# Optimization experiments

Measured on AMD Instinct MI355X. Metric: run time of the kernel, lower is better.

The kernel has to match this reference:

```python
import jax, jax.numpy as jnp
import numpy as np

N = 50000      # nodes
E = 400000     # edges
F = 64         # feature_size
H = 4          # heads
D = 16         # embedding_size (per-head dim)
HD = H * D     # concat hidden = 64
ED = 16        # edge_dim
L = 3          # model_layers (extra TransformerConv layers)
DN = 256       # dense_neurons
G = 128        # number of graphs in the batch
SCALE = float(1.0 / np.sqrt(D))


def setup_inputs() -> dict:
    key = jax.random.key(0)
    ks = jax.random.split(key, 40)

    def w(k, shape, fan_in):
        return jax.random.normal(k, shape, jnp.float32) / np.float32(np.sqrt(fan_in))

    inp = {}
    inp["x"] = jax.random.normal(ks[0], (N, F), jnp.float32)
    inp["edge_attr"] = jax.random.normal(ks[1], (E, ED), jnp.float32)
    inp["edge_index"] = jax.random.randint(ks[2], (2, E), 0, N)
    inp["batch"] = jnp.sort(jax.random.randint(ks[3], (N,), 0, G))

    # conv1: feature_size -> heads*embedding
    inp["Wq0"] = w(ks[4], (F, HD), F); inp["bq0"] = jnp.zeros((HD,), jnp.float32)
    inp["Wk0"] = w(ks[5], (F, HD), F); inp["bk0"] = jnp.zeros((HD,), jnp.float32)
    inp["Wv0"] = w(ks[6], (F, HD), F); inp["bv0"] = jnp.zeros((HD,), jnp.float32)
    inp["We0"] = w(ks[7], (ED, HD), ED)                      # lin_edge, no bias
    inp["Ws0"] = w(ks[8], (F, HD), F); inp["bs0"] = jnp.zeros((HD,), jnp.float32)  # lin_skip
    inp["Wb0"] = w(ks[9], (3 * HD, 1), 3 * HD)               # lin_beta, no bias

    # stacked layers 1..L: heads*embedding -> heads*embedding
    inp["Wq"] = w(ks[10], (L, HD, HD), HD); inp["bq"] = jnp.zeros((L, HD), jnp.float32)
    inp["Wk"] = w(ks[11], (L, HD, HD), HD); inp["bk"] = jnp.zeros((L, HD), jnp.float32)
    inp["Wv"] = w(ks[12], (L, HD, HD), HD); inp["bv"] = jnp.zeros((L, HD), jnp.float32)
    inp["We"] = w(ks[13], (L, ED, HD), ED)
    inp["Ws"] = w(ks[14], (L, HD, HD), HD); inp["bs"] = jnp.zeros((L, HD), jnp.float32)
    inp["Wb"] = w(ks[15], (L, 3 * HD, 1), 3 * HD)

    # MLP head: Linear(2*HD -> DN), Linear(DN -> 1)
    inp["Wlin"] = w(ks[16], (2 * HD, DN), 2 * HD); inp["blin"] = jnp.zeros((DN,), jnp.float32)
    inp["Wout"] = w(ks[17], (DN, 1), DN); inp["bout"] = jnp.zeros((1,), jnp.float32)
    return inp


def _tconv(x, edge_attr, src, dst, Wq, bq, Wk, bk, Wv, bv, We, Ws, bs, Wb):
    """PyG TransformerConv (concat=True, beta=True, edge_dim), eval mode (no dropout)."""
    n = x.shape[0]
    q = (x @ Wq + bq).reshape(n, H, D)
    k = (x @ Wk + bk).reshape(n, H, D)
    v = (x @ Wv + bv).reshape(n, H, D)
    e = (edge_attr @ We).reshape(-1, H, D)
    ke = k[src] + e                                   # [E,H,D] keys with edge feats
    ve = v[src] + e                                   # [E,H,D] values with edge feats
    logits = jnp.einsum('ehd,ehd->eh', q[dst], ke) * SCALE
    # segment softmax over incoming edges of each target node
    m = jax.ops.segment_max(logits, dst, num_segments=n)
    p = jnp.exp(logits - m[dst])
    s = jax.ops.segment_sum(p, dst, num_segments=n)
    a = p / (s[dst] + 1e-16)                          # [E,H]
    agg = jax.ops.segment_sum(a[:, :, None] * ve, dst, num_segments=n).reshape(n, HD)
    skip = x @ Ws + bs                                # root/skip transform
    beta = jax.nn.sigmoid(jnp.concatenate([agg, skip, agg - skip], axis=-1) @ Wb)
    return beta * skip + (1.0 - beta) * agg


def reference(x, edge_attr, edge_index, batch,
              Wq0, bq0, Wk0, bk0, Wv0, bv0, We0, Ws0, bs0, Wb0,
              Wq, bq, Wk, bk, Wv, bv, We, Ws, bs, Wb,
              Wlin, blin, Wout, bout):
    src, dst = edge_index[0], edge_index[1]
    h = jax.nn.relu(_tconv(x, edge_attr, src, dst,
                           Wq0, bq0, Wk0, bk0, Wv0, bv0, We0, Ws0, bs0, Wb0))
    for i in range(L):
        h = jax.nn.relu(_tconv(h, edge_attr, src, dst,
                               Wq[i], bq[i], Wk[i], bk[i], Wv[i], bv[i],
                               We[i], Ws[i], bs[i], Wb[i]))
    # global max pool (gmp) and global mean pool (gap)
    cnt = jax.ops.segment_sum(jnp.ones((h.shape[0],), h.dtype), batch, num_segments=G)
    gmax = jax.ops.segment_max(h, batch, num_segments=G)
    gmax = jnp.where(cnt[:, None] > 0, gmax, 0.0)
    gmean = jax.ops.segment_sum(h, batch, num_segments=G) / jnp.maximum(cnt[:, None], 1.0)
    z = jnp.concatenate([gmax, gmean], axis=-1) @ Wlin + blin
    return jax.nn.sigmoid(z @ Wout + bout)
```

## Files before the change

### kernel.cpp

```cpp
#include <hip/hip_runtime.h>
#include <math.h>

#define SCALEF 0.25f
#define LOG2E  1.4426950408889634f

typedef __attribute__((ext_vector_type(8))) short short8;
typedef __attribute__((ext_vector_type(4))) float f32x4;

__device__ __forceinline__ unsigned short f2bf(float x) {
  unsigned u = __float_as_uint(x);
  unsigned r = u + 0x7FFFu + ((u >> 16) & 1u);
  return (unsigned short)(r >> 16);
}
__device__ __forceinline__ float bf2f(unsigned short h) {
  return __uint_as_float(((unsigned)h) << 16);
}

__global__ void k_hist(const int* __restrict__ dst, int* __restrict__ counts, int E) {
  int i = blockIdx.x * 256 + threadIdx.x;
  if (i < E) atomicAdd(&counts[dst[i]], 1);
}

__global__ __launch_bounds__(1024) void k_scan1(const int* __restrict__ counts,
                                                int* __restrict__ excl,
                                                int* __restrict__ bsums, int n) {
  __shared__ int sd[1024];
  int t = threadIdx.x;
  int i = blockIdx.x * 1024 + t;
  int v = (i < n) ? counts[i] : 0;
  sd[t] = v;
  __syncthreads();
  for (int off = 1; off < 1024; off <<= 1) {
    int x = (t >= off) ? sd[t - off] : 0;
    __syncthreads();
    sd[t] += x;
    __syncthreads();
  }
  if (i < n) excl[i] = sd[t] - v;
  if (t == 1023) bsums[blockIdx.x] = sd[1023];
}

__global__ __launch_bounds__(64) void k_scan2(int* bsums, int nb) {
  const int lane = threadIdx.x;
  int v = (lane < nb) ? bsums[lane] : 0;
  const int orig = v;
  for (int off = 1; off < 64; off <<= 1) {
    int u = __shfl_up(v, off, 64);
    if (lane >= off) v += u;
  }
  if (lane < nb) bsums[lane] = v - orig;
}

__global__ __launch_bounds__(1024) void k_scan3(int* __restrict__ rowptr, int* __restrict__ cursor,
                                                const int* __restrict__ bsums, int n, int Etot) {
  int i = blockIdx.x * 1024 + threadIdx.x;
  if (i < n) { int v = rowptr[i] + bsums[blockIdx.x]; rowptr[i] = v; cursor[i] = v; }
  if (i == 0) rowptr[n] = Etot;
}

__global__ void k_scatperm(const int* __restrict__ esrc, const int* __restrict__ edst,
                           const float* __restrict__ EA, int* __restrict__ cursor,
                           int* __restrict__ esrcp, unsigned short* __restrict__ EAp, int E) {
  int i = blockIdx.x * 256 + threadIdx.x;
  if (i >= E) return;
  const int pos = atomicAdd(&cursor[edst[i]], 1);
  esrcp[pos] = esrc[i] * 256;
  const float4* s4 = (const float4*)(EA + ((size_t)i << 4));
  float4 a = s4[0], b = s4[1], c = s4[2], d = s4[3];
  union { unsigned short us[16]; uint4 u4[2]; } o;
  o.us[0] = f2bf(a.x); o.us[1] = f2bf(a.y); o.us[2] = f2bf(a.z); o.us[3] = f2bf(a.w);
  o.us[4] = f2bf(b.x); o.us[5] = f2bf(b.y); o.us[6] = f2bf(b.z); o.us[7] = f2bf(b.w);
  o.us[8] = f2bf(c.x); o.us[9] = f2bf(c.y); o.us[10] = f2bf(c.z); o.us[11] = f2bf(c.w);
  o.us[12] = f2bf(d.x); o.us[13] = f2bf(d.y); o.us[14] = f2bf(d.z); o.us[15] = f2bf(d.w);
  uint4* d4 = (uint4*)(EAp + ((size_t)pos << 4));
  d4[0] = o.u4[0]; d4[1] = o.u4[1];
}

__global__ __launch_bounds__(256) void k_wqt(
    const float* __restrict__ Wq0, const float* __restrict__ bq0, const float* __restrict__ We0,
    const float* __restrict__ Wq, const float* __restrict__ bq, const float* __restrict__ We,
    float* __restrict__ Wqt, float* __restrict__ bqt) {
  const int l = blockIdx.x;
  const float* wq = (l == 0) ? Wq0 : Wq + (l - 1) * 4096;
  const float* bv = (l == 0) ? bq0 : bq + (l - 1) * 64;
  const float* we = (l == 0) ? We0 : We + (l - 1) * 1024;
  float* out  = Wqt + l * 4096;
  float* outb = bqt + l * 64;
  const int t = threadIdx.x;
  const int r = t >> 2;
  const int hh = t & 3;
  float wqr[16];
  #pragma unroll
  for (int d = 0; d < 16; ++d) wqr[d] = wq[r * 64 + hh * 16 + d];
  #pragma unroll
  for (int bb = 0; bb < 16; ++bb) {
    float s = 0.f;
    #pragma unroll
    for (int d = 0; d < 16; ++d) s += wqr[d] * we[bb * 64 + hh * 16 + d];
    out[r * 64 + hh * 16 + bb] = s * SCALEF;
  }
  if (r == 0) {
    #pragma unroll
    for (int bb = 0; bb < 16; ++bb) {
      float s = 0.f;
      #pragma unroll
      for (int d = 0; d < 16; ++d) s += bv[hh * 16 + d] * we[bb * 64 + hh * 16 + d];
      outb[hh * 16 + bb] = s * SCALEF;
    }
  }
}

__global__ void k_prep(
    const float* __restrict__ x, unsigned short* __restrict__ xb, int n16,
    const float* __restrict__ Wq0, const float* __restrict__ Wk0, const float* __restrict__ Wv0,
    const float* __restrict__ Ws0,
    const float* __restrict__ Wq, const float* __restrict__ Wk, const float* __restrict__ Wv,
    const float* __restrict__ Ws, const float* __restrict__ Wqt,
    const float* __restrict__ bq0, const float* __restrict__ bk0, const float* __restrict__ bv0,
    const float* __restrict__ bs0,
    const float* __restrict__ bq, const float* __restrict__ bk, const float* __restrict__ bv,
    const float* __restrict__ bs, const float* __restrict__ bqt,
    unsigned short* __restrict__ WT, float* __restrict__ bcat) {
  const int id = blockIdx.x * 256 + threadIdx.x;
  if (id < n16) {
    float4 v = ((const float4*)x)[id];
    ushort4 o;
    o.x = f2bf(v.x); o.y = f2bf(v.y); o.z = f2bf(v.z); o.w = f2bf(v.w);
    ((ushort4*)xb)[id] = o;
  }
  if (id < 4 * 5 * 4096) {
    const int l = id / 20480;
    const int rem = id - l * 20480;
    const int mat = rem >> 12;
    const int idx = rem & 4095;
    const int k = idx >> 6;
    const int c = idx & 63;
    float v;
    if (mat == 0)      v = (l == 0) ? Wq0[idx] : Wq[(l - 1) * 4096 + idx];
    else if (mat == 1) v = (l == 0) ? Wk0[idx] : Wk[(l - 1) * 4096 + idx];
    else if (mat == 2) v = (l == 0) ? Wv0[idx] : Wv[(l - 1) * 4096 + idx];
    else if (mat == 3) v = (l == 0) ? Ws0[idx] : Ws[(l - 1) * 4096 + idx];
    else               v = Wqt[l * 4096 + idx];
    WT[(size_t)(l * 5 + mat) * 4096 + c * 64 + k] = f2bf(v);
    if (k == 0) {
      float b;
      if (mat == 0)      b = (l == 0) ? bq0[c] : bq[(l - 1) * 64 + c];
      else if (mat == 1) b = (l == 0) ? bk0[c] : bk[(l - 1) * 64 + c];
      else if (mat == 2) b = (l == 0) ? bv0[c] : bv[(l - 1) * 64 + c];
      else if (mat == 3) b = (l == 0) ? bs0[c] : bs[(l - 1) * 64 + c];
      else               b = bqt[l * 64 + c];
      bcat[(l * 5 + mat) * 64 + c] = b;
    }
  }
}

__device__ __forceinline__ void mat_gemm(const unsigned short* __restrict__ wb,
                                         const short8 a0, const short8 a1,
                                         f32x4 acc[4]) {
  #pragma unroll
  for (int cf = 0; cf < 4; ++cf) {
    short8 b0 = *(const short8*)(wb + cf * 1024);
    short8 b1 = *(const short8*)(wb + cf * 1024 + 32);
    acc[cf] = __builtin_amdgcn_mfma_f32_16x16x32_bf16(a0, b0, acc[cf], 0, 0, 0);
    acc[cf] = __builtin_amdgcn_mfma_f32_16x16x32_bf16(a1, b1, acc[cf], 0, 0, 0);
  }
}

__global__ __launch_bounds__(256) void k_linm(
    const unsigned short* __restrict__ Xb, const unsigned short* __restrict__ WT,
    const float* __restrict__ bcat,
    unsigned int* __restrict__ QTu, unsigned int* __restrict__ KVu,
    unsigned short* __restrict__ Sb, int n) {
  const int lane = threadIdx.x & 63;
  const int tile = blockIdx.x * 4 + (threadIdx.x >> 6);
  const int ntr = n >> 4;
  if (tile >= ntr) return;
  const int r0 = tile << 4;
  const int c15 = lane & 15;
  const int kg = lane >> 4;
  const int rbase = r0 + kg * 4;

  const unsigned short* xrow = Xb + (size_t)(r0 + c15) * 64 + kg * 8;
  const short8 a0 = *(const short8*)(xrow);
  const short8 a1 = *(const short8*)(xrow + 32);
  const f32x4 z = {0.f, 0.f, 0.f, 0.f};

  {
    f32x4 aK[4] = {z, z, z, z}, aV[4] = {z, z, z, z};
    mat_gemm(WT + (1 << 12) + (size_t)c15 * 64 + kg * 8, a0, a1, aK);
    mat_gemm(WT + (2 << 12) + (size_t)c15 * 64 + kg * 8, a0, a1, aV);
    #pragma unroll
    for (int cf = 0; cf < 4; ++cf) {
      const float bk_ = bcat[1 * 64 + cf * 16 + c15];
      const float bv_ = bcat[2 * 64 + cf * 16 + c15];
      #pragma unroll
      for (int reg = 0; reg < 4; ++reg) {
        const unsigned pk = f2bf(aK[cf][reg] + bk_);
        const unsigned pv = f2bf(aV[cf][reg] + bv_);
        KVu[(size_t)(rbase + reg) * 64 + cf * 16 + c15] = pk | (pv << 16);
      }
    }
  }

  {
    f32x4 aQ[4] = {z, z, z, z}, aT[4] = {z, z, z, z};
    mat_gemm(WT + (0 << 12) + (size_t)c15 * 64 + kg * 8, a0, a1, aQ);
    mat_gemm(WT + ((size_t)4 << 12) + (size_t)c15 * 64 + kg * 8, a0, a1, aT);
    #pragma unroll
    for (int cf = 0; cf < 4; ++cf) {
      const float bq_ = bcat[0 * 64 + cf * 16 + c15];
      const float bt_ = bcat[4 * 64 + cf * 16 + c15];
      #pragma unroll
      for (int reg = 0; reg < 4; ++reg) {
        const unsigned pq = f2bf(aQ[cf][reg] + bq_);
        const unsigned pt = f2bf(aT[cf][reg] + bt_);
        QTu[(size_t)(rbase + reg) * 64 + cf * 16 + c15] = pq | (pt << 16);
      }
    }
  }

  {
    f32x4 aS[4] = {z, z, z, z};
    mat_gemm(WT + ((size_t)3 << 12) + (size_t)c15 * 64 + kg * 8, a0, a1, aS);
    #pragma unroll
    for (int cf = 0; cf < 4; ++cf) {
      const float bs_ = bcat[3 * 64 + cf * 16 + c15];
      #pragma unroll
      for (int reg = 0; reg < 4; ++reg) {
        Sb[(size_t)(rbase + reg) * 64 + cf * 16 + c15] = f2bf(aS[cf][reg] + bs_);
      }
    }
  }
}

#define DPPRED(pl) do {                                                           \
    pl += __int_as_float(__builtin_amdgcn_update_dpp(0, __float_as_int(pl),       \
                                                     0xB1, 0xF, 0xF, true));      \
    pl += __int_as_float(__builtin_amdgcn_update_dpp(0, __float_as_int(pl),       \
                                                     0x4E, 0xF, 0xF, true));      \
    pl += __int_as_float(__builtin_amdgcn_update_dpp(0, __float_as_int(pl),       \
                                                     0x124, 0xF, 0xF, true));     \
    pl += __int_as_float(__builtin_amdgcn_update_dpp(0, __float_as_int(pl),       \
                                                     0x128, 0xF, 0xF, true));     \
  } while (0)

#define LOADST(KV, EE, jj) do {                                           \
    int jc_ = (jj) < mc ? (jj) : mc - 1;                                  \
    int off_ = __builtin_amdgcn_readlane(snv, jc_);                       \
    KV = *(const unsigned int*)(kvbase + off_);                           \
    EE = eabase[(size_t)(c0 + jc_) << 4];                                 \
  } while (0)

#define COMPUTE(KV, EE, jj) do {                                          \
    if ((jj) < mc) {                                                      \
      const float ef = bf2f(EE);                                          \
      const float kf = __uint_as_float(KV << 16);                         \
      const float vf = __uint_as_float(KV & 0xFFFF0000u);                 \
      float pl = qv * kf + tl * ef;                                       \
      DPPRED(pl);                                                         \
      const float p = exp2f(pl);                                          \
      ssum += p;                                                          \
      accv += p * vf;                                                     \
      accw += p * ef;                                                     \
    }                                                                     \
  } while (0)

__global__ __launch_bounds__(128, 8) void k_attn(
    const unsigned int* __restrict__ QTu, const unsigned int* __restrict__ KVu,
    const unsigned short* __restrict__ Sb, const unsigned short* __restrict__ EAp,
    const int* __restrict__ esrcp, const int* __restrict__ rowptr,
    const float* __restrict__ We, const float* __restrict__ Wb,
    unsigned short* __restrict__ Hout, int n) {
  const int t = threadIdx.x;
  const int lane = t & 63;
  const int node = blockIdx.x * 2 + (t >> 6);
  if (node >= n) return;

  const unsigned int qt = QTu[(size_t)node * 64 + lane];
  const float qv = __uint_as_float(qt << 16) * (SCALEF * LOG2E);
  const float tl = __uint_as_float(qt & 0xFFFF0000u) * LOG2E;
  const int r0 = rowptr[node], r1 = rowptr[node + 1];

  const char* kvbase = (const char*)KVu + 4 * lane;
  const unsigned short* eabase = EAp + (lane & 15);

  float ssum = 0.f, accv = 0.f, accw = 0.f;

  for (int c0 = r0; c0 < r1; c0 += 64) {
    const int mc = min(64, r1 - c0);
    int snv = 0;
    if (lane < mc) snv = esrcp[c0 + lane];

    unsigned int kvA, kvB, kvC, kvD;
    unsigned short eA, eB, eC, eD;
    LOADST(kvA, eA, 0);
    LOADST(kvB, eB, 1);
    LOADST(kvC, eC, 2);
    LOADST(kvD, eD, 3);

    for (int j = 0; j < mc; j += 4) {
      COMPUTE(kvA, eA, j);     LOADST(kvA, eA, j + 4);
      COMPUTE(kvB, eB, j + 1); LOADST(kvB, eB, j + 5);
      COMPUTE(kvC, eC, j + 2); LOADST(kvC, eC, j + 6);
      COMPUTE(kvD, eD, j + 3); LOADST(kvD, eD, j + 7);
    }
  }

  float agg = accv;
  #pragma unroll
  for (int j = 0; j < 16; ++j) {
    const float wj = __shfl(accw, (lane & 48) | j, 64);
    agg += wj * We[j * 64 + lane];
  }
  agg /= (ssum + 1e-16f);

  const float sk = bf2f(Sb[(size_t)node * 64 + lane]);
  float contrib = agg * Wb[lane] + sk * Wb[64 + lane] + (agg - sk) * Wb[128 + lane];
  #pragma unroll
  for (int off = 1; off < 64; off <<= 1) contrib += __shfl_xor(contrib, off, 64);
  const float beta = 1.f / (1.f + __expf(-contrib));
  const float o = beta * sk + (1.f - beta) * agg;
  Hout[(size_t)node * 64 + lane] = f2bf(fmaxf(o, 0.f));
}

__global__ __launch_bounds__(256) void k_poolmlp(const unsigned short* __restrict__ Hf,
    const int* __restrict__ batch,
    const float* __restrict__ Wlin, const float* __restrict__ blin,
    const float* __restrict__ Wout, const float* __restrict__ bout,
    float* __restrict__ out, int n) {
  const int g = blockIdx.x;
  const int t = threadIdx.x;
  const int lane = t & 63;
  const int w = t >> 6;

  int a = 0, b = n;
  while (a < b) { int mid = (a + b) >> 1; if (batch[mid] < g) a = mid + 1; else b = mid; }
  const int lo = a;
  b = n;
  while (a < b) { int mid = (a + b) >> 1; if (batch[mid] < g + 1) a = mid + 1; else b = mid; }
  const int hi = a;

  float vmax = -1e30f, vsum = 0.f;
  for (int i = lo + w; i < hi; i += 4) {
    const float v = bf2f(Hf[(size_t)i * 64 + lane]);
    vmax = fmaxf(vmax, v);
    vsum += v;
  }
  __shared__ float smax[4][64], ssum[4][64];
  __shared__ float cat[128];
  smax[w][lane] = vmax;
  ssum[w][lane] = vsum;
  __syncthreads();
  if (w == 0) {
    const float mx = fmaxf(fmaxf(smax[0][lane], smax[1][lane]),
                           fmaxf(smax[2][lane], smax[3][lane]));
    const float sm = ssum[0][lane] + ssum[1][lane] + ssum[2][lane] + ssum[3][lane];
    const int cnt = hi - lo;
    cat[lane]      = (cnt > 0) ? mx : 0.f;
    cat[64 + lane] = sm / fmaxf((float)cnt, 1.f);
  }
  __syncthreads();

  float acc = blin[t];
  for (int j = 0; j < 128; ++j) acc += cat[j] * Wlin[j * 256 + t];
  float p = acc * Wout[t];
  #pragma unroll
  for (int off = 1; off < 64; off <<= 1) p += __shfl_xor(p, off, 64);
  __shared__ float red[4];
  if ((t & 63) == 0) red[t >> 6] = p;
  __syncthreads();
  if (t == 0) {
    const float z = red[0] + red[1] + red[2] + red[3] + bout[0];
    out[g] = 1.f / (1.f + __expf(-z));
  }
}

extern "C" void kernel_launch(void* const* d_in, const int* in_sizes, int n_in,
                              void* d_out, int out_size, void* d_ws, size_t ws_size,
                              hipStream_t stream) {
  const float* x     = (const float*)d_in[0];
  const float* ea    = (const float*)d_in[1];
  const int*   eidx  = (const int*)d_in[2];
  const int*   batch = (const int*)d_in[3];
  const float *Wq0 = (const float*)d_in[4],  *bq0 = (const float*)d_in[5];
  const float *Wk0 = (const float*)d_in[6],  *bk0 = (const float*)d_in[7];
  const float *Wv0 = (const float*)d_in[8],  *bv0 = (const float*)d_in[9];
  const float *We0 = (const float*)d_in[10];
  const float *Ws0 = (const float*)d_in[11], *bs0 = (const float*)d_in[12];
  const float *Wb0 = (const float*)d_in[13];
  const float *Wq  = (const float*)d_in[14], *bq  = (const float*)d_in[15];
  const float *Wk  = (const float*)d_in[16], *bk  = (const float*)d_in[17];
  const float *Wv  = (const float*)d_in[18], *bv  = (const float*)d_in[19];
  const float *We  = (const float*)d_in[20];
  const float *Ws  = (const float*)d_in[21], *bs  = (const float*)d_in[22];
  const float *Wb  = (const float*)d_in[23];
  const float *Wlin = (const float*)d_in[24], *blin = (const float*)d_in[25];
  const float *Wout = (const float*)d_in[26], *bout = (const float*)d_in[27];

  const int N = in_sizes[0] / 64;
  const int E = in_sizes[2] / 2;
  const int G = out_size;
  const int* esrc = eidx;
  const int* edst = eidx + E;

  char* wsp = (char*)d_ws;
  auto alloc = [&](size_t bytes) -> void* {
    void* p = (void*)wsp;
    wsp += (bytes + 255) & ~(size_t)255;
    return p;
  };
  unsigned int* QTu = (unsigned int*)alloc((size_t)N * 64 * 4);
  unsigned int* KVu = (unsigned int*)alloc((size_t)N * 64 * 4);
  unsigned short* Sb16 = (unsigned short*)alloc((size_t)N * 64 * 2);
  unsigned short* Hb16 = (unsigned short*)alloc((size_t)N * 64 * 2);
  unsigned short* Xb16 = (unsigned short*)alloc((size_t)N * 64 * 2);
  int* counts  = (int*)alloc((size_t)N * 4);
  int* rowptr  = (int*)alloc((size_t)(N + 1) * 4);
  int* cursor  = (int*)alloc((size_t)N * 4);
  int* bsums   = (int*)alloc(1024 * 4);
  int* esrcp   = (int*)alloc((size_t)E * 4);
  unsigned short* EAp = (unsigned short*)alloc((size_t)E * 16 * 2);
  float* Wqt   = (float*)alloc(4 * 4096 * 4);
  float* bqt   = (float*)alloc(4 * 64 * 4);
  unsigned short* WT = (unsigned short*)alloc(4 * 5 * 4096 * 2);
  float* bcat  = (float*)alloc(4 * 5 * 64 * 4);

  const int gridE = (E + 255) / 256;
  const int NB1 = (N + 1023) / 1024;
  hipMemsetAsync(counts, 0, (size_t)N * 4, stream);
  k_hist<<<gridE, 256, 0, stream>>>(edst, counts, E);
  k_scan1<<<NB1, 1024, 0, stream>>>(counts, rowptr, bsums, N);
  k_scan2<<<1, 64, 0, stream>>>(bsums, NB1);
  k_scan3<<<NB1, 1024, 0, stream>>>(rowptr, cursor, bsums, N, E);
  k_scatperm<<<gridE, 256, 0, stream>>>(esrc, edst, ea, cursor, esrcp, EAp, E);
  k_wqt<<<4, 256, 0, stream>>>(Wq0, bq0, We0, Wq, bq, We, Wqt, bqt);
  k_prep<<<(N * 16 + 255) / 256, 256, 0, stream>>>(
      x, Xb16, N * 16,
      Wq0, Wk0, Wv0, Ws0, Wq, Wk, Wv, Ws, Wqt,
      bq0, bk0, bv0, bs0, bq, bk, bv, bs, bqt, WT, bcat);

  const int gridLinM = ((N >> 4) + 3) / 4;
  const int gridAttn = (N + 1) / 2;
  for (int l = 0; l < 4; ++l) {
    const float* we_ = (l == 0) ? We0 : We + (l - 1) * 1024;
    const float* wb_ = (l == 0) ? Wb0 : Wb + (l - 1) * 192;
    const unsigned short* xin = (l == 0) ? Xb16 : Hb16;
    k_linm<<<gridLinM, 256, 0, stream>>>(xin, WT + (size_t)l * 20480, bcat + l * 320,
                                         QTu, KVu, Sb16, N);
    k_attn<<<gridAttn, 128, 0, stream>>>(QTu, KVu, Sb16, EAp, esrcp, rowptr,
                                         we_, wb_, Hb16, N);
  }

  k_poolmlp<<<G, 256, 0, stream>>>(Hb16, batch, Wlin, blin, Wout, bout,
                                   (float*)d_out, N);
}
```

Before: 355.6 us.

## Fold scan2 and wqt kernels into neighbors, move edge-attr permute into prep

Merges the block-sum scan into k_scan3, with each block rescanning the 64 block sums, and folds the Wq·We precompute into k_prep, removing two kernel launches. The scatter now writes (src, original edge id) pairs, and k_prep gathers and converts the edge attributes in sorted order, so the EAp writes become coalesced and the reads become gathers. The attention inner loop drops its branch and masks out-of-range edges with a large negative exponent offset. In exchange, the index array doubles in size and attention reads 8-byte entries to get the source index.

```diff
diff --git a/kernel.cpp b/kernel.cpp
--- a/kernel.cpp
+++ b/kernel.cpp
@@ -40,74 +40,33 @@
   if (t == 1023) bsums[blockIdx.x] = sd[1023];
 }
 
-__global__ __launch_bounds__(64) void k_scan2(int* bsums, int nb) {
-  const int lane = threadIdx.x;
-  int v = (lane < nb) ? bsums[lane] : 0;
-  const int orig = v;
-  for (int off = 1; off < 64; off <<= 1) {
-    int u = __shfl_up(v, off, 64);
-    if (lane >= off) v += u;
-  }
-  if (lane < nb) bsums[lane] = v - orig;
-}
-
 __global__ __launch_bounds__(1024) void k_scan3(int* __restrict__ rowptr, int* __restrict__ cursor,
-                                                const int* __restrict__ bsums, int n, int Etot) {
-  int i = blockIdx.x * 1024 + threadIdx.x;
-  if (i < n) { int v = rowptr[i] + bsums[blockIdx.x]; rowptr[i] = v; cursor[i] = v; }
+                                                const int* __restrict__ bsums, int nb,
+                                                int n, int Etot) {
+  __shared__ int boff_s;
+  const int t = threadIdx.x;
+  if (t < 64) {
+    int v = (t < nb) ? bsums[t] : 0;
+    int incl = v;
+    for (int off = 1; off < 64; off <<= 1) {
+      int u = __shfl_up(incl, off, 64);
+      if (t >= off) incl += u;
+    }
+    if (t == blockIdx.x) boff_s = incl - v;
+  }
+  __syncthreads();
+  const int boff = boff_s;
+  int i = blockIdx.x * 1024 + t;
+  if (i < n) { int v = rowptr[i] + boff; rowptr[i] = v; cursor[i] = v; }
   if (i == 0) rowptr[n] = Etot;
 }
 
 __global__ void k_scatperm(const int* __restrict__ esrc, const int* __restrict__ edst,
-                           const float* __restrict__ EA, int* __restrict__ cursor,
-                           int* __restrict__ esrcp, unsigned short* __restrict__ EAp, int E) {
+                           int* __restrict__ cursor, int2* __restrict__ eidx2, int E) {
   int i = blockIdx.x * 256 + threadIdx.x;
   if (i >= E) return;
   const int pos = atomicAdd(&cursor[edst[i]], 1);
-  esrcp[pos] = esrc[i] * 256;
-  const float4* s4 = (const float4*)(EA + ((size_t)i << 4));
-  float4 a = s4[0], b = s4[1], c = s4[2], d = s4[3];
-  union { unsigned short us[16]; uint4 u4[2]; } o;
-  o.us[0] = f2bf(a.x); o.us[1] = f2bf(a.y); o.us[2] = f2bf(a.z); o.us[3] = f2bf(a.w);
-  o.us[4] = f2bf(b.x); o.us[5] = f2bf(b.y); o.us[6] = f2bf(b.z); o.us[7] = f2bf(b.w);
-  o.us[8] = f2bf(c.x); o.us[9] = f2bf(c.y); o.us[10] = f2bf(c.z); o.us[11] = f2bf(c.w);
-  o.us[12] = f2bf(d.x); o.us[13] = f2bf(d.y); o.us[14] = f2bf(d.z); o.us[15] = f2bf(d.w);
-  uint4* d4 = (uint4*)(EAp + ((size_t)pos << 4));
-  d4[0] = o.u4[0]; d4[1] = o.u4[1];
-}
-
-__global__ __launch_bounds__(256) void k_wqt(
-    const float* __restrict__ Wq0, const float* __restrict__ bq0, const float* __restrict__ We0,
-    const float* __restrict__ Wq, const float* __restrict__ bq, const float* __restrict__ We,
-    float* __restrict__ Wqt, float* __restrict__ bqt) {
-  const int l = blockIdx.x;
-  const float* wq = (l == 0) ? Wq0 : Wq + (l - 1) * 4096;
-  const float* bv = (l == 0) ? bq0 : bq + (l - 1) * 64;
-  const float* we = (l == 0) ? We0 : We + (l - 1) * 1024;
-  float* out  = Wqt + l * 4096;
-  float* outb = bqt + l * 64;
-  const int t = threadIdx.x;
-  const int r = t >> 2;
-  const int hh = t & 3;
-  float wqr[16];
-  #pragma unroll
-  for (int d = 0; d < 16; ++d) wqr[d] = wq[r * 64 + hh * 16 + d];
-  #pragma unroll
-  for (int bb = 0; bb < 16; ++bb) {
-    float s = 0.f;
-    #pragma unroll
-    for (int d = 0; d < 16; ++d) s += wqr[d] * we[bb * 64 + hh * 16 + d];
-    out[r * 64 + hh * 16 + bb] = s * SCALEF;
-  }
-  if (r == 0) {
-    #pragma unroll
-    for (int bb = 0; bb < 16; ++bb) {
-      float s = 0.f;
-      #pragma unroll
-      for (int d = 0; d < 16; ++d) s += bv[hh * 16 + d] * we[bb * 64 + hh * 16 + d];
-      outb[hh * 16 + bb] = s * SCALEF;
-    }
-  }
+  eidx2[pos] = make_int2(esrc[i] * 256, i);
 }
 
 __global__ void k_prep(
@@ -115,18 +74,33 @@
     const float* __restrict__ Wq0, const float* __restrict__ Wk0, const float* __restrict__ Wv0,
     const float* __restrict__ Ws0,
     const float* __restrict__ Wq, const float* __restrict__ Wk, const float* __restrict__ Wv,
-    const float* __restrict__ Ws, const float* __restrict__ Wqt,
+    const float* __restrict__ Ws,
     const float* __restrict__ bq0, const float* __restrict__ bk0, const float* __restrict__ bv0,
     const float* __restrict__ bs0,
     const float* __restrict__ bq, const float* __restrict__ bk, const float* __restrict__ bv,
-    const float* __restrict__ bs, const float* __restrict__ bqt,
-    unsigned short* __restrict__ WT, float* __restrict__ bcat) {
+    const float* __restrict__ bs,
+    const float* __restrict__ We0, const float* __restrict__ We,
+    unsigned short* __restrict__ WT, float* __restrict__ bcat,
+    const float* __restrict__ EA, const int2* __restrict__ eidx2,
+    unsigned short* __restrict__ EAp, int E) {
   const int id = blockIdx.x * 256 + threadIdx.x;
   if (id < n16) {
     float4 v = ((const float4*)x)[id];
     ushort4 o;
     o.x = f2bf(v.x); o.y = f2bf(v.y); o.z = f2bf(v.z); o.w = f2bf(v.w);
     ((ushort4*)xb)[id] = o;
+  }
+  if (id < E) {
+    const int eid = eidx2[id].y;
+    const float4* s4 = (const float4*)(EA + ((size_t)eid << 4));
+    float4 a = s4[0], b = s4[1], c = s4[2], d = s4[3];
+    union { unsigned short us[16]; uint4 u4[2]; } o;
+    o.us[0] = f2bf(a.x); o.us[1] = f2bf(a.y); o.us[2] = f2bf(a.z); o.us[3] = f2bf(a.w);
+    o.us[4] = f2bf(b.x); o.us[5] = f2bf(b.y); o.us[6] = f2bf(b.z); o.us[7] = f2bf(b.w);
+    o.us[8] = f2bf(c.x); o.us[9] = f2bf(c.y); o.us[10] = f2bf(c.z); o.us[11] = f2bf(c.w);
+    o.us[12] = f2bf(d.x); o.us[13] = f2bf(d.y); o.us[14] = f2bf(d.z); o.us[15] = f2bf(d.w);
+    uint4* d4 = (uint4*)(EAp + ((size_t)id << 4));
+    d4[0] = o.u4[0]; d4[1] = o.u4[1];
   }
   if (id < 4 * 5 * 4096) {
     const int l = id / 20480;
@@ -135,12 +109,20 @@
     const int idx = rem & 4095;
     const int k = idx >> 6;
     const int c = idx & 63;
+    const float* we = (l == 0) ? We0 : We + (l - 1) * 1024;
     float v;
     if (mat == 0)      v = (l == 0) ? Wq0[idx] : Wq[(l - 1) * 4096 + idx];
     else if (mat == 1) v = (l == 0) ? Wk0[idx] : Wk[(l - 1) * 4096 + idx];
     else if (mat == 2) v = (l == 0) ? Wv0[idx] : Wv[(l - 1) * 4096 + idx];
     else if (mat == 3) v = (l == 0) ? Ws0[idx] : Ws[(l - 1) * 4096 + idx];
-    else               v = Wqt[l * 4096 + idx];
+    else {
+      const float* wq = (l == 0) ? Wq0 : Wq + (l - 1) * 4096;
+      const int hb = c & 48;
+      float s = 0.f;
+      #pragma unroll
+      for (int d = 0; d < 16; ++d) s += wq[k * 64 + hb + d] * we[(c & 15) * 64 + hb + d];
+      v = s * SCALEF;
+    }
     WT[(size_t)(l * 5 + mat) * 4096 + c * 64 + k] = f2bf(v);
     if (k == 0) {
       float b;
@@ -148,7 +130,14 @@
       else if (mat == 1) b = (l == 0) ? bk0[c] : bk[(l - 1) * 64 + c];
       else if (mat == 2) b = (l == 0) ? bv0[c] : bv[(l - 1) * 64 + c];
       else if (mat == 3) b = (l == 0) ? bs0[c] : bs[(l - 1) * 64 + c];
-      else               b = bqt[l * 64 + c];
+      else {
+        const float* bqv = (l == 0) ? bq0 : bq + (l - 1) * 64;
+        const int hb = c & 48;
+        float s = 0.f;
+        #pragma unroll
+        for (int d = 0; d < 16; ++d) s += bqv[hb + d] * we[(c & 15) * 64 + hb + d];
+        b = s * SCALEF;
+      }
       bcat[(l * 5 + mat) * 64 + c] = b;
     }
   }
@@ -252,23 +241,22 @@
   } while (0)
 
 #define COMPUTE(KV, EE, jj) do {                                          \
-    if ((jj) < mc) {                                                      \
-      const float ef = bf2f(EE);                                          \
-      const float kf = __uint_as_float(KV << 16);                         \
-      const float vf = __uint_as_float(KV & 0xFFFF0000u);                 \
-      float pl = qv * kf + tl * ef;                                       \
-      DPPRED(pl);                                                         \
-      const float p = exp2f(pl);                                          \
-      ssum += p;                                                          \
-      accv += p * vf;                                                     \
-      accw += p * ef;                                                     \
-    }                                                                     \
+    const float sel = ((jj) < mc) ? 0.f : -1e30f;                         \
+    const float ef = bf2f(EE);                                            \
+    const float kf = __uint_as_float(KV << 16);                           \
+    const float vf = __uint_as_float(KV & 0xFFFF0000u);                   \
+    float pl = qv * kf + tl * ef;                                         \
+    DPPRED(pl);                                                           \
+    const float p = exp2f(pl + sel);                                      \
+    ssum += p;                                                            \
+    accv += p * vf;                                                       \
+    accw += p * ef;                                                       \
   } while (0)
 
 __global__ __launch_bounds__(128, 8) void k_attn(
     const unsigned int* __restrict__ QTu, const unsigned int* __restrict__ KVu,
     const unsigned short* __restrict__ Sb, const unsigned short* __restrict__ EAp,
-    const int* __restrict__ esrcp, const int* __restrict__ rowptr,
+    const int2* __restrict__ eidx2, const int* __restrict__ rowptr,
     const float* __restrict__ We, const float* __restrict__ Wb,
     unsigned short* __restrict__ Hout, int n) {
   const int t = threadIdx.x;
@@ -289,7 +277,7 @@
   for (int c0 = r0; c0 < r1; c0 += 64) {
     const int mc = min(64, r1 - c0);
     int snv = 0;
-    if (lane < mc) snv = esrcp[c0 + lane];
+    if (lane < mc) snv = eidx2[c0 + lane].x;
 
     unsigned int kvA, kvB, kvC, kvD;
     unsigned short eA, eB, eC, eD;
@@ -418,10 +406,8 @@
   int* rowptr  = (int*)alloc((size_t)(N + 1) * 4);
   int* cursor  = (int*)alloc((size_t)N * 4);
   int* bsums   = (int*)alloc(1024 * 4);
-  int* esrcp   = (int*)alloc((size_t)E * 4);
+  int2* eidx2  = (int2*)alloc((size_t)E * 8);
   unsigned short* EAp = (unsigned short*)alloc((size_t)E * 16 * 2);
-  float* Wqt   = (float*)alloc(4 * 4096 * 4);
-  float* bqt   = (float*)alloc(4 * 64 * 4);
   unsigned short* WT = (unsigned short*)alloc(4 * 5 * 4096 * 2);
   float* bcat  = (float*)alloc(4 * 5 * 64 * 4);
 
@@ -430,14 +416,14 @@
   hipMemsetAsync(counts, 0, (size_t)N * 4, stream);
   k_hist<<<gridE, 256, 0, stream>>>(edst, counts, E);
   k_scan1<<<NB1, 1024, 0, stream>>>(counts, rowptr, bsums, N);
-  k_scan2<<<1, 64, 0, stream>>>(bsums, NB1);
-  k_scan3<<<NB1, 1024, 0, stream>>>(rowptr, cursor, bsums, N, E);
-  k_scatperm<<<gridE, 256, 0, stream>>>(esrc, edst, ea, cursor, esrcp, EAp, E);
-  k_wqt<<<4, 256, 0, stream>>>(Wq0, bq0, We0, Wq, bq, We, Wqt, bqt);
-  k_prep<<<(N * 16 + 255) / 256, 256, 0, stream>>>(
-      x, Xb16, N * 16,
-      Wq0, Wk0, Wv0, Ws0, Wq, Wk, Wv, Ws, Wqt,
-      bq0, bk0, bv0, bs0, bq, bk, bv, bs, bqt, WT, bcat);
+  k_scan3<<<NB1, 1024, 0, stream>>>(rowptr, cursor, bsums, NB1, N, E);
+  k_scatperm<<<gridE, 256, 0, stream>>>(esrc, edst, cursor, eidx2, E);
+  const int n16 = N * 16;
+  k_prep<<<(n16 + 255) / 256, 256, 0, stream>>>(
+      x, Xb16, n16,
+      Wq0, Wk0, Wv0, Ws0, Wq, Wk, Wv, Ws,
+      bq0, bk0, bv0, bs0, bq, bk, bv, bs,
+      We0, We, WT, bcat, ea, eidx2, EAp, E);
 
   const int gridLinM = ((N >> 4) + 3) / 4;
   const int gridAttn = (N + 1) / 2;
@@ -447,7 +433,7 @@
     const unsigned short* xin = (l == 0) ? Xb16 : Hb16;
     k_linm<<<gridLinM, 256, 0, stream>>>(xin, WT + (size_t)l * 20480, bcat + l * 320,
                                          QTu, KVu, Sb16, N);
-    k_attn<<<gridAttn, 128, 0, stream>>>(QTu, KVu, Sb16, EAp, esrcp, rowptr,
+    k_attn<<<gridAttn, 128, 0, stream>>>(QTu, KVu, Sb16, EAp, eidx2, rowptr,
                                          we_, wb_, Hb16, N);
   }
 
```

After: 352.1 us (median of 2 runs). No clear change (-1.0%).
